# Kernel optimization log

Measured on AMD Instinct MI355X. Metric: run time of the kernel, lower is better.

Reference implementation:

```python
import jax, jax.numpy as jnp
import numpy as np

D_MODEL = 2048
NUM_EXPERTS = 64
TOP_K = 2


def setup_inputs() -> dict:
    key = jax.random.key(0)
    k1, k2 = jax.random.split(key)
    x = jax.random.normal(k1, (4, 4096, D_MODEL), dtype=jnp.float32)
    # nn.Linear(d_model, num_experts) weight: [num_experts, d_model]
    W_gate = jax.random.normal(k2, (NUM_EXPERTS, D_MODEL), dtype=jnp.float32) * (1.0 / np.sqrt(D_MODEL))
    return {"x": x, "W_gate": W_gate}


def reference(x, W_gate):
    # logits: [b, s, e]
    logits = jnp.einsum("bsd,ed->bse", x, W_gate)
    probs = jax.nn.softmax(logits, axis=-1)
    expert_weights, expert_indices = jax.lax.top_k(probs, TOP_K)  # [b, s, k]
    expert_weights = expert_weights / jnp.sum(expert_weights, axis=-1, keepdims=True)
    return expert_indices, expert_weights
```

## Files before the change

### kernel.cpp

```cpp
#include <hip/hip_runtime.h>
#include <math.h>

#define NTOK 16384
#define DK   2048
#define NEXP 64

typedef float f32x4 __attribute__((ext_vector_type(4)));
typedef int   i32x4 __attribute__((ext_vector_type(4)));
typedef short s16x8 __attribute__((ext_vector_type(8)));

__device__ __forceinline__ unsigned short f2bf(float f) {
    union { float f; unsigned u; } v; v.f = f;
    unsigned r = (v.u + 0x7FFFu + ((v.u >> 16) & 1u)) >> 16;
    return (unsigned short)r;
}
__device__ __forceinline__ float bf2f(unsigned short h) {
    union { unsigned u; float f; } v; v.u = ((unsigned)h) << 16;
    return v.f;
}

__global__ __launch_bounds__(256) void wsplit_pack(const float* __restrict__ Wg,
                                                   unsigned short* __restrict__ ws) {
    const int t  = blockIdx.x * 256 + threadIdx.x;
    const int e  = t >> 8;
    const int k  = (t & 255) * 8;
    const int R  = k >> 5;
    const int g  = (k >> 3) & 3;
    const int rr = e & 15;
    const int n  = e >> 4;
    const int lane = g * 16 + rr;

    const float* src = Wg + (size_t)e * DK + k;
    unsigned short p0[8], p1[8], p2[8];
    #pragma unroll
    for (int j = 0; j < 8; ++j) {
        const float f = src[j];
        p0[j] = f2bf(f);  const float r1 = f - bf2f(p0[j]);
        p1[j] = f2bf(r1); const float r2 = r1 - bf2f(p1[j]);
        p2[j] = f2bf(r2);
    }
    const size_t base = (((size_t)R * 4 + n) * 3) * 512 + (size_t)lane * 8;
    *(s16x8*)(ws + base)        = *(s16x8*)p0;
    *(s16x8*)(ws + base + 512)  = *(s16x8*)p1;
    *(s16x8*)(ws + base + 1024) = *(s16x8*)p2;
}

__device__ __forceinline__ void gload_lds16(const float* src, float* dst) {
    __builtin_amdgcn_global_load_lds(
        (const __attribute__((address_space(1))) void*)src,
        (__attribute__((address_space(3))) void*)dst, 16, 0, 0);
}

__device__ __forceinline__ unsigned cvtpk(float lo, float hi) {
    unsigned r;
    asm("v_cvt_pk_bf16_f32 %0, %1, %2" : "=v"(r) : "v"(lo), "v"(hi));
    return r;
}

#define SPLIT2(F0, F1, O0, O1, O2) { \
    const unsigned q0 = cvtpk((F0), (F1)); \
    const float s0 = (F0) - __builtin_bit_cast(float, q0 << 16); \
    const float s1 = (F1) - __builtin_bit_cast(float, q0 & 0xFFFF0000u); \
    const unsigned q1 = cvtpk(s0, s1); \
    const float t0 = s0 - __builtin_bit_cast(float, q1 << 16); \
    const float t1 = s1 - __builtin_bit_cast(float, q1 & 0xFFFF0000u); \
    O0 = (int)q0; O1 = (int)q1; O2 = (int)cvtpk(t0, t1); }

#define STAGE_X(c, BUF) { \
    _Pragma("unroll") for (int it = 0; it < 4; ++it) \
        gload_lds16(xsrc + (size_t)it * 8 * DK + (size_t)(c) * 32, \
                    &xs[w][BUF][it * 256]); }

#define ISSUE_B(BS, R) { \
    _Pragma("unroll") for (int n = 0; n < 4; ++n) \
        _Pragma("unroll") for (int p = 0; p < 3; ++p) \
            BS[n][p] = *(const i32x4*)(wbase + ((size_t)(R) * 12 + n * 3 + p) * 512); }

#define CONV_LDS(BUF) { \
    _Pragma("unroll") for (int m = 0; m < 2; ++m) { \
        const int row = rr + 16 * m; \
        const int sw  = row & 7; \
        const float4 xa0 = *(const float4*)&xs[w][BUF][row * 32 + (((g * 2 + 0) ^ sw) << 2)]; \
        const float4 xa1 = *(const float4*)&xs[w][BUF][row * 32 + (((g * 2 + 1) ^ sw) << 2)]; \
        SPLIT2(xa0.x, xa0.y, A[m][0].x, A[m][1].x, A[m][2].x); \
        SPLIT2(xa0.z, xa0.w, A[m][0].y, A[m][1].y, A[m][2].y); \
        SPLIT2(xa1.x, xa1.y, A[m][0].z, A[m][1].z, A[m][2].z); \
        SPLIT2(xa1.z, xa1.w, A[m][0].w, A[m][1].w, A[m][2].w); } }

#define MFMA_TERM(pa, pb, BS) { \
    _Pragma("unroll") for (int m = 0; m < 2; ++m) \
        _Pragma("unroll") for (int n = 0; n < 4; ++n) \
            acc[m][n] = __builtin_amdgcn_mfma_f32_16x16x32_bf16( \
                __builtin_bit_cast(s16x8, A[m][pa]), \
                __builtin_bit_cast(s16x8, BS[n][pb]), acc[m][n], 0, 0, 0); }

#define MFMA_ALL(BS) \
    MFMA_TERM(0, 0, BS) MFMA_TERM(0, 1, BS) MFMA_TERM(1, 0, BS) \
    MFMA_TERM(1, 1, BS) MFMA_TERM(0, 2, BS) MFMA_TERM(2, 0, BS)

#define PHASE(c, NCNT, DO_X) { \
    ISSUE_B(BS, R0 + (c)); \
    asm volatile("s_waitcnt vmcnt(" #NCNT ")" ::: "memory"); \
    __builtin_amdgcn_sched_barrier(0); \
    CONV_LDS((c) & 1); \
    MFMA_ALL(BS); \
    if (DO_X) STAGE_X((c) + 2, (c) & 1); \
    __builtin_amdgcn_sched_barrier(0); }

__global__ __launch_bounds__(512, 4) void topk_router_kernel(
    const float* __restrict__ x,
    const unsigned short* __restrict__ ws,
    float* __restrict__ out)
{
    __shared__ float smem[16640];
    float (*xs)[2][1024] = (float (*)[2][1024])smem;

    const int tid  = threadIdx.x;
    const int w    = tid >> 6;
    const int lane = tid & 63;
    const int rr   = lane & 15;
    const int g    = lane >> 4;
    const int tok0 = blockIdx.x * 32;
    const int R0   = w * 8;

    const int lt = lane >> 3;
    const int lq = lane & 7;
    const float* xsrc = x + (size_t)(tok0 + lt) * DK + w * 256 + ((lq ^ lt) * 4);
    const unsigned short* wbase = ws + (size_t)lane * 8;

    f32x4 acc[2][4];
    #pragma unroll
    for (int m = 0; m < 2; ++m)
        #pragma unroll
        for (int n = 0; n < 4; ++n) acc[m][n] = (f32x4){0.f, 0.f, 0.f, 0.f};

    i32x4 BS[4][3];
    i32x4 A[2][3];

    STAGE_X(0, 0);
    STAGE_X(1, 1);

    PHASE(0, 16, 1);
    PHASE(1, 16, 1);
    PHASE(2, 16, 1);
    PHASE(3, 16, 1);
    PHASE(4, 16, 1);
    PHASE(5, 16, 1);
    PHASE(6, 16, 0);
    PHASE(7, 12, 0);

    __syncthreads();
    {
        float* lg = smem;
        #pragma unroll
        for (int m = 0; m < 2; ++m)
            #pragma unroll
            for (int n = 0; n < 4; ++n)
                #pragma unroll
                for (int r = 0; r < 4; ++r)
                    lg[(w * 32 + m * 16 + g * 4 + r) * 65 + n * 16 + rr]
                        = acc[m][n][r];
    }
    __syncthreads();

    #pragma unroll 1
    for (int t = 0; t < 4; ++t) {
        const int tok = w * 4 + t;
        float v = 0.f;
        #pragma unroll
        for (int p = 0; p < 8; ++p) v += smem[(p * 32 + tok) * 65 + lane];

        float m1 = v; int i1 = lane;
        #pragma unroll
        for (int off = 32; off > 0; off >>= 1) {
            float ov = __shfl_xor(m1, off);
            int   oi = __shfl_xor(i1, off);
            if (ov > m1 || (ov == m1 && oi < i1)) { m1 = ov; i1 = oi; }
        }
        float m2 = (lane == i1) ? -INFINITY : v; int i2 = lane;
        #pragma unroll
        for (int off = 32; off > 0; off >>= 1) {
            float ov = __shfl_xor(m2, off);
            int   oi = __shfl_xor(i2, off);
            if (ov > m2 || (ov == m2 && oi < i2)) { m2 = ov; i2 = oi; }
        }

        if (lane == 0) {
            const int gtok = tok0 + tok;
            const float e  = expf(m2 - m1);
            const float w1 = 1.0f / (1.0f + e);
            const float w2 = e / (1.0f + e);
            out[gtok * 2 + 0] = (float)i1;
            out[gtok * 2 + 1] = (float)i2;
            out[NTOK * 2 + gtok * 2 + 0] = w1;
            out[NTOK * 2 + gtok * 2 + 1] = w2;
        }
    }
}

extern "C" void kernel_launch(void* const* d_in, const int* in_sizes, int n_in,
                              void* d_out, int out_size, void* d_ws, size_t ws_size,
                              hipStream_t stream) {
    const float* x  = (const float*)d_in[0];
    const float* Wg = (const float*)d_in[1];
    float* out = (float*)d_out;
    unsigned short* ws = (unsigned short*)d_ws;
    hipLaunchKernelGGL(wsplit_pack, dim3(64), dim3(256), 0, stream, Wg, ws);
    hipLaunchKernelGGL(topk_router_kernel, dim3(NTOK / 32), dim3(512), 0, stream,
                       x, ws, out);
}
```

Before: 50.19 us.

## Process 64 tokens per block with 4-way K split and 64-wide x stages

The block now handles 64 tokens split into two token groups of 32, and the K dimension is divided across 4 waves instead of 8. Each wave stages 64-wide K chunks of x into LDS (double-buffered, 16-way XOR swizzle) and runs two MFMA sub-steps per stage. The weight pack layout is changed to match the new K partition. The aim is to halve the number of blocks and the cross-wave partial-sum reduction work relative to tokens processed. The cost is double the LDS per block and lower occupancy (launch bounds 2 instead of 4).

```diff
diff --git a/kernel.cpp b/kernel.cpp
--- a/kernel.cpp
+++ b/kernel.cpp
@@ -24,7 +24,8 @@
     const int t  = blockIdx.x * 256 + threadIdx.x;
     const int e  = t >> 8;
     const int k  = (t & 255) * 8;
-    const int R  = k >> 5;
+    const int q  = k >> 9;
+    const int c  = (k >> 5) & 15;
     const int g  = (k >> 3) & 3;
     const int rr = e & 15;
     const int n  = e >> 4;
@@ -39,7 +40,7 @@
         p1[j] = f2bf(r1); const float r2 = r1 - bf2f(p1[j]);
         p2[j] = f2bf(r2);
     }
-    const size_t base = (((size_t)R * 4 + n) * 3) * 512 + (size_t)lane * 8;
+    const size_t base = ((((size_t)q * 16 + c) * 4 + n) * 3) * 512 + (size_t)lane * 8;
     *(s16x8*)(ws + base)        = *(s16x8*)p0;
     *(s16x8*)(ws + base + 512)  = *(s16x8*)p1;
     *(s16x8*)(ws + base + 1024) = *(s16x8*)p2;
@@ -66,22 +67,23 @@
     const float t1 = s1 - __builtin_bit_cast(float, q1 & 0xFFFF0000u); \
     O0 = (int)q0; O1 = (int)q1; O2 = (int)cvtpk(t0, t1); }
 
-#define STAGE_X(c, BUF) { \
-    _Pragma("unroll") for (int it = 0; it < 4; ++it) \
-        gload_lds16(xsrc + (size_t)it * 8 * DK + (size_t)(c) * 32, \
-                    &xs[w][BUF][it * 256]); }
-
-#define ISSUE_B(BS, R) { \
+#define STAGE_X(s, BUF) { \
+    _Pragma("unroll") for (int it = 0; it < 8; ++it) { \
+        const int row = it * 4 + lt; \
+        gload_lds16(xsrc + (size_t)(it * 4) * DK + (size_t)(s) * 64 \
+                         + ((lgq ^ (row & 15)) * 4), \
+                    &xs[w][BUF][it * 256]); } }
+
+#define ISSUE_B(BS, c) { \
     _Pragma("unroll") for (int n = 0; n < 4; ++n) \
         _Pragma("unroll") for (int p = 0; p < 3; ++p) \
-            BS[n][p] = *(const i32x4*)(wbase + ((size_t)(R) * 12 + n * 3 + p) * 512); }
-
-#define CONV_LDS(BUF) { \
+            BS[n][p] = *(const i32x4*)(wbase + ((size_t)(c) * 12 + n * 3 + p) * 512); }
+
+#define CONV_LDS(BUF, SB) { \
     _Pragma("unroll") for (int m = 0; m < 2; ++m) { \
         const int row = rr + 16 * m; \
-        const int sw  = row & 7; \
-        const float4 xa0 = *(const float4*)&xs[w][BUF][row * 32 + (((g * 2 + 0) ^ sw) << 2)]; \
-        const float4 xa1 = *(const float4*)&xs[w][BUF][row * 32 + (((g * 2 + 1) ^ sw) << 2)]; \
+        const float4 xa0 = *(const float4*)&xs[w][BUF][row * 64 + ((((SB) * 8 + g * 2 + 0) ^ rr) << 2)]; \
+        const float4 xa1 = *(const float4*)&xs[w][BUF][row * 64 + ((((SB) * 8 + g * 2 + 1) ^ rr) << 2)]; \
         SPLIT2(xa0.x, xa0.y, A[m][0].x, A[m][1].x, A[m][2].x); \
         SPLIT2(xa0.z, xa0.w, A[m][0].y, A[m][1].y, A[m][2].y); \
         SPLIT2(xa1.x, xa1.y, A[m][0].z, A[m][1].z, A[m][2].z); \
@@ -98,35 +100,39 @@
     MFMA_TERM(0, 0, BS) MFMA_TERM(0, 1, BS) MFMA_TERM(1, 0, BS) \
     MFMA_TERM(1, 1, BS) MFMA_TERM(0, 2, BS) MFMA_TERM(2, 0, BS)
 
-#define PHASE(c, NCNT, DO_X) { \
-    ISSUE_B(BS, R0 + (c)); \
+#define SUPER(s, NCNT, DO_X) { \
+    ISSUE_B(BS, (s) * 2); \
     asm volatile("s_waitcnt vmcnt(" #NCNT ")" ::: "memory"); \
     __builtin_amdgcn_sched_barrier(0); \
-    CONV_LDS((c) & 1); \
+    CONV_LDS((s) & 1, 0); \
     MFMA_ALL(BS); \
-    if (DO_X) STAGE_X((c) + 2, (c) & 1); \
+    ISSUE_B(BS, (s) * 2 + 1); \
+    CONV_LDS((s) & 1, 1); \
+    MFMA_ALL(BS); \
+    if (DO_X) STAGE_X((s) + 2, (s) & 1); \
     __builtin_amdgcn_sched_barrier(0); }
 
-__global__ __launch_bounds__(512, 4) void topk_router_kernel(
+__global__ __launch_bounds__(512, 2) void topk_router_kernel(
     const float* __restrict__ x,
     const unsigned short* __restrict__ ws,
     float* __restrict__ out)
 {
-    __shared__ float smem[16640];
-    float (*xs)[2][1024] = (float (*)[2][1024])smem;
+    __shared__ float smem[32768];
+    float (*xs)[2][2048] = (float (*)[2][2048])smem;
 
     const int tid  = threadIdx.x;
     const int w    = tid >> 6;
     const int lane = tid & 63;
+    const int tg   = w >> 2;
+    const int kq   = w & 3;
     const int rr   = lane & 15;
     const int g    = lane >> 4;
-    const int tok0 = blockIdx.x * 32;
-    const int R0   = w * 8;
-
-    const int lt = lane >> 3;
-    const int lq = lane & 7;
-    const float* xsrc = x + (size_t)(tok0 + lt) * DK + w * 256 + ((lq ^ lt) * 4);
-    const unsigned short* wbase = ws + (size_t)lane * 8;
+    const int tok0w = blockIdx.x * 64 + tg * 32;
+
+    const int lt  = lane >> 4;
+    const int lgq = lane & 15;
+    const float* xsrc = x + (size_t)(tok0w + lt) * DK + kq * 512;
+    const unsigned short* wbase = ws + (size_t)kq * 98304 + (size_t)lane * 8;
 
     f32x4 acc[2][4];
     #pragma unroll
@@ -140,14 +146,14 @@
     STAGE_X(0, 0);
     STAGE_X(1, 1);
 
-    PHASE(0, 16, 1);
-    PHASE(1, 16, 1);
-    PHASE(2, 16, 1);
-    PHASE(3, 16, 1);
-    PHASE(4, 16, 1);
-    PHASE(5, 16, 1);
-    PHASE(6, 16, 0);
-    PHASE(7, 12, 0);
+    SUPER(0, 20, 1);
+    SUPER(1, 20, 1);
+    SUPER(2, 20, 1);
+    SUPER(3, 20, 1);
+    SUPER(4, 20, 1);
+    SUPER(5, 20, 1);
+    SUPER(6, 20, 0);
+    SUPER(7, 12, 0);
 
     __syncthreads();
     {
@@ -158,17 +164,17 @@
             for (int n = 0; n < 4; ++n)
                 #pragma unroll
                 for (int r = 0; r < 4; ++r)
-                    lg[(w * 32 + m * 16 + g * 4 + r) * 65 + n * 16 + rr]
+                    lg[((kq * 64) + tg * 32 + m * 16 + g * 4 + r) * 65 + n * 16 + rr]
                         = acc[m][n][r];
     }
     __syncthreads();
 
     #pragma unroll 1
-    for (int t = 0; t < 4; ++t) {
-        const int tok = w * 4 + t;
+    for (int t = 0; t < 8; ++t) {
+        const int tok = w * 8 + t;
         float v = 0.f;
         #pragma unroll
-        for (int p = 0; p < 8; ++p) v += smem[(p * 32 + tok) * 65 + lane];
+        for (int p = 0; p < 4; ++p) v += smem[(p * 64 + tok) * 65 + lane];
 
         float m1 = v; int i1 = lane;
         #pragma unroll
@@ -186,7 +192,7 @@
         }
 
         if (lane == 0) {
-            const int gtok = tok0 + tok;
+            const int gtok = blockIdx.x * 64 + tok;
             const float e  = expf(m2 - m1);
             const float w1 = 1.0f / (1.0f + e);
             const float w2 = e / (1.0f + e);
@@ -206,6 +212,6 @@
     float* out = (float*)d_out;
     unsigned short* ws = (unsigned short*)d_ws;
     hipLaunchKernelGGL(wsplit_pack, dim3(64), dim3(256), 0, stream, Wg, ws);
-    hipLaunchKernelGGL(topk_router_kernel, dim3(NTOK / 32), dim3(512), 0, stream,
+    hipLaunchKernelGGL(topk_router_kernel, dim3(NTOK / 64), dim3(512), 0, stream,
                        x, ws, out);
 }
```

Measured after the change: 49.67 us. Within noise of the previous version (-1.0%).

## Double token tile per block to 64 and reuse gate-weight fragments across rows

Applied to the files above, without the earlier changes.

Each block now handles 64 tokens instead of 32, so every loaded bf16-split weight fragment feeds four 16-row MFMA groups instead of two. This halves the number of weight fragment loads per token. The x split into bf16 parts is now done one row-group at a time to save A registers. The cost is larger accumulators (16 per wave), doubled LDS staging and a launch bound of one block per CU. The grid halves to 256 blocks, which lowers occupancy and latency hiding on the 256-CU part.

```diff
diff --git a/kernel.cpp b/kernel.cpp
--- a/kernel.cpp
+++ b/kernel.cpp
@@ -67,7 +67,7 @@
     O0 = (int)q0; O1 = (int)q1; O2 = (int)cvtpk(t0, t1); }
 
 #define STAGE_X(c, BUF) { \
-    _Pragma("unroll") for (int it = 0; it < 4; ++it) \
+    _Pragma("unroll") for (int it = 0; it < 8; ++it) \
         gload_lds16(xsrc + (size_t)it * 8 * DK + (size_t)(c) * 32, \
                     &xs[w][BUF][it * 256]); }
 
@@ -76,51 +76,53 @@
         _Pragma("unroll") for (int p = 0; p < 3; ++p) \
             BS[n][p] = *(const i32x4*)(wbase + ((size_t)(R) * 12 + n * 3 + p) * 512); }
 
-#define CONV_LDS(BUF) { \
-    _Pragma("unroll") for (int m = 0; m < 2; ++m) { \
-        const int row = rr + 16 * m; \
-        const int sw  = row & 7; \
-        const float4 xa0 = *(const float4*)&xs[w][BUF][row * 32 + (((g * 2 + 0) ^ sw) << 2)]; \
-        const float4 xa1 = *(const float4*)&xs[w][BUF][row * 32 + (((g * 2 + 1) ^ sw) << 2)]; \
-        SPLIT2(xa0.x, xa0.y, A[m][0].x, A[m][1].x, A[m][2].x); \
-        SPLIT2(xa0.z, xa0.w, A[m][0].y, A[m][1].y, A[m][2].y); \
-        SPLIT2(xa1.x, xa1.y, A[m][0].z, A[m][1].z, A[m][2].z); \
-        SPLIT2(xa1.z, xa1.w, A[m][0].w, A[m][1].w, A[m][2].w); } }
-
-#define MFMA_TERM(pa, pb, BS) { \
-    _Pragma("unroll") for (int m = 0; m < 2; ++m) \
-        _Pragma("unroll") for (int n = 0; n < 4; ++n) \
-            acc[m][n] = __builtin_amdgcn_mfma_f32_16x16x32_bf16( \
-                __builtin_bit_cast(s16x8, A[m][pa]), \
-                __builtin_bit_cast(s16x8, BS[n][pb]), acc[m][n], 0, 0, 0); }
-
-#define MFMA_ALL(BS) \
-    MFMA_TERM(0, 0, BS) MFMA_TERM(0, 1, BS) MFMA_TERM(1, 0, BS) \
-    MFMA_TERM(1, 1, BS) MFMA_TERM(0, 2, BS) MFMA_TERM(2, 0, BS)
-
-#define PHASE(c, NCNT, DO_X) { \
+#define CONV_M(BUF, m_) { \
+    const int row_ = rr + 16 * (m_); \
+    const int sw_  = rr & 7; \
+    const float4 xa0 = *(const float4*)&xs[w][BUF][row_ * 32 + (((g * 2 + 0) ^ sw_) << 2)]; \
+    const float4 xa1 = *(const float4*)&xs[w][BUF][row_ * 32 + (((g * 2 + 1) ^ sw_) << 2)]; \
+    SPLIT2(xa0.x, xa0.y, A[0].x, A[1].x, A[2].x); \
+    SPLIT2(xa0.z, xa0.w, A[0].y, A[1].y, A[2].y); \
+    SPLIT2(xa1.x, xa1.y, A[0].z, A[1].z, A[2].z); \
+    SPLIT2(xa1.z, xa1.w, A[0].w, A[1].w, A[2].w); }
+
+#define MFMA1(Aa, Bb, Cc) __builtin_amdgcn_mfma_f32_16x16x32_bf16( \
+    __builtin_bit_cast(s16x8, Aa), __builtin_bit_cast(s16x8, Bb), Cc, 0, 0, 0)
+
+#define MFMA_M(m_) { \
+    _Pragma("unroll") for (int n = 0; n < 4; ++n) { \
+        acc[m_][n] = MFMA1(A[0], BS[n][0], acc[m_][n]); \
+        acc[m_][n] = MFMA1(A[0], BS[n][1], acc[m_][n]); \
+        acc[m_][n] = MFMA1(A[1], BS[n][0], acc[m_][n]); \
+        acc[m_][n] = MFMA1(A[1], BS[n][1], acc[m_][n]); \
+        acc[m_][n] = MFMA1(A[0], BS[n][2], acc[m_][n]); \
+        acc[m_][n] = MFMA1(A[2], BS[n][0], acc[m_][n]); } }
+
+#define ROUND(c, NCNT, DO_X) { \
     ISSUE_B(BS, R0 + (c)); \
     asm volatile("s_waitcnt vmcnt(" #NCNT ")" ::: "memory"); \
     __builtin_amdgcn_sched_barrier(0); \
-    CONV_LDS((c) & 1); \
-    MFMA_ALL(BS); \
+    CONV_M((c) & 1, 0) MFMA_M(0) \
+    CONV_M((c) & 1, 1) MFMA_M(1) \
+    CONV_M((c) & 1, 2) MFMA_M(2) \
+    CONV_M((c) & 1, 3) MFMA_M(3) \
     if (DO_X) STAGE_X((c) + 2, (c) & 1); \
     __builtin_amdgcn_sched_barrier(0); }
 
-__global__ __launch_bounds__(512, 4) void topk_router_kernel(
+__global__ __launch_bounds__(512, 1) void topk_router_kernel(
     const float* __restrict__ x,
     const unsigned short* __restrict__ ws,
     float* __restrict__ out)
 {
-    __shared__ float smem[16640];
-    float (*xs)[2][1024] = (float (*)[2][1024])smem;
+    __shared__ float smem[33280];
+    float (*xs)[2][2048] = (float (*)[2][2048])smem;
 
     const int tid  = threadIdx.x;
     const int w    = tid >> 6;
     const int lane = tid & 63;
     const int rr   = lane & 15;
     const int g    = lane >> 4;
-    const int tok0 = blockIdx.x * 32;
+    const int tok0 = blockIdx.x * 64;
     const int R0   = w * 8;
 
     const int lt = lane >> 3;
@@ -128,47 +130,47 @@
     const float* xsrc = x + (size_t)(tok0 + lt) * DK + w * 256 + ((lq ^ lt) * 4);
     const unsigned short* wbase = ws + (size_t)lane * 8;
 
-    f32x4 acc[2][4];
+    f32x4 acc[4][4];
     #pragma unroll
-    for (int m = 0; m < 2; ++m)
+    for (int m = 0; m < 4; ++m)
         #pragma unroll
         for (int n = 0; n < 4; ++n) acc[m][n] = (f32x4){0.f, 0.f, 0.f, 0.f};
 
     i32x4 BS[4][3];
-    i32x4 A[2][3];
+    i32x4 A[3];
 
     STAGE_X(0, 0);
     STAGE_X(1, 1);
 
-    PHASE(0, 16, 1);
-    PHASE(1, 16, 1);
-    PHASE(2, 16, 1);
-    PHASE(3, 16, 1);
-    PHASE(4, 16, 1);
-    PHASE(5, 16, 1);
-    PHASE(6, 16, 0);
-    PHASE(7, 12, 0);
+    ROUND(0, 20, 1);
+    ROUND(1, 20, 1);
+    ROUND(2, 20, 1);
+    ROUND(3, 20, 1);
+    ROUND(4, 20, 1);
+    ROUND(5, 20, 1);
+    ROUND(6, 20, 0);
+    ROUND(7, 12, 0);
 
     __syncthreads();
     {
         float* lg = smem;
         #pragma unroll
-        for (int m = 0; m < 2; ++m)
+        for (int m = 0; m < 4; ++m)
             #pragma unroll
             for (int n = 0; n < 4; ++n)
                 #pragma unroll
                 for (int r = 0; r < 4; ++r)
-                    lg[(w * 32 + m * 16 + g * 4 + r) * 65 + n * 16 + rr]
+                    lg[(w * 64 + m * 16 + g * 4 + r) * 65 + n * 16 + rr]
                         = acc[m][n][r];
     }
     __syncthreads();
 
     #pragma unroll 1
-    for (int t = 0; t < 4; ++t) {
-        const int tok = w * 4 + t;
+    for (int t = 0; t < 8; ++t) {
+        const int tok = w * 8 + t;
         float v = 0.f;
         #pragma unroll
-        for (int p = 0; p < 8; ++p) v += smem[(p * 32 + tok) * 65 + lane];
+        for (int p = 0; p < 8; ++p) v += smem[(p * 64 + tok) * 65 + lane];
 
         float m1 = v; int i1 = lane;
         #pragma unroll
@@ -206,6 +208,6 @@
     float* out = (float*)d_out;
     unsigned short* ws = (unsigned short*)d_ws;
     hipLaunchKernelGGL(wsplit_pack, dim3(64), dim3(256), 0, stream, Wg, ws);
-    hipLaunchKernelGGL(topk_router_kernel, dim3(NTOK / 32), dim3(512), 0, stream,
+    hipLaunchKernelGGL(topk_router_kernel, dim3(NTOK / 64), dim3(512), 0, stream,
                        x, ws, out);
 }
```

Measured after the change: 48.16 us. 1.04x faster.
